# Optimization experiments

Hardware: AMD Instinct MI355X
Metric: run time of the kernel (lower is better)

## Reference

```python
import jax, jax.numpy as jnp
import numpy as np
import math

B, N, D, H, BS = 1, 2048, 1024, 16, 256  # batch, seq, d_model, heads, block_size


def setup_inputs() -> dict:
    key = jax.random.key(0)
    ks = jax.random.split(key, 8)
    s = 0.02  # init scale for projection weights
    return {
        "x": jax.random.normal(ks[0], (B, N, D), jnp.float32),
        "distance_bias": jax.random.uniform(ks[1], (N, N), dtype=jnp.float32),
        "Wq": jax.random.normal(ks[2], (D, D), jnp.float32) * s,
        "bq": jnp.zeros((D,), jnp.float32),
        "Wk": jax.random.normal(ks[3], (D, D), jnp.float32) * s,
        "bk": jnp.zeros((D,), jnp.float32),
        "Wv": jax.random.normal(ks[4], (D, D), jnp.float32) * s,
        "bv": jnp.zeros((D,), jnp.float32),
        "Wo": jax.random.normal(ks[5], (D, D), jnp.float32) * s,
        "bo": jnp.zeros((D,), jnp.float32),
    }


def reference(x, distance_bias, Wq, bq, Wk, bk, Wv, bv, Wo, bo):
    Bm, Nm, Dm = x.shape
    dk = Dm // H
    scale = 1.0 / math.sqrt(dk)
    nb = Nm // BS  # number of blocks along sequence

    def proj(W, b):
        # torch Linear: x @ W.T + b, then split heads -> [B, H, N, dk]
        return (x @ W.T + b).reshape(Bm, Nm, H, dk).transpose(0, 2, 1, 3)

    Q, K, V = proj(Wq, bq), proj(Wk, bk), proj(Wv, bv)

    # scores with toroidal bias subtracted (matches `scores - bias_block`)
    scores = jnp.einsum('bhqd,bhkd->bhqk', Q, K) * scale - distance_bias[None, None]
    # view as [B, H, n_qblk, BS, n_kblk, BS] and softmax PER (q-block, k-block)
    s6 = scores.reshape(Bm, H, nb, BS, nb, BS)
    w = jax.nn.softmax(s6, axis=-1)  # softmax over keys within each kv block

    Vb = V.reshape(Bm, H, nb, BS, dk)
    # sum over all kv blocks of (per-block softmax) @ V_block
    num = jnp.einsum('bhqsnk,bhnkd->bhqsd', w, Vb)  # [B,H,nb,BS,dk]
    # accumulated normalizer = sum of per-block softmax weights over all kv blocks
    norm = jnp.sum(w, axis=(4, 5))  # [B,H,nb,BS]
    O = num / (norm[..., None] + 1e-8)

    O = O.reshape(Bm, H, Nm, dk).transpose(0, 2, 1, 3).reshape(Bm, Nm, Dm)
    return O @ Wo.T + bo
```

## Files before the change

kernel.cpp:

```cpp
#include <hip/hip_runtime.h>
#include <hip/hip_fp16.h>

typedef _Float16 half8 __attribute__((ext_vector_type(8)));
typedef _Float16 half4v __attribute__((ext_vector_type(4)));
typedef float f32x4 __attribute__((ext_vector_type(4)));

#define NSEQ 2048
#define DMOD 1024
#define NHEAD 16
#define DK 64

#define GLOAD_LDS16(gp, lp) __builtin_amdgcn_global_load_lds(                 \
    (const __attribute__((address_space(1))) void*)(gp),                      \
    (__attribute__((address_space(3))) void*)(lp), 16, 0, 0)

#define WAIT_VM(n) (0xF70 | (n))


__global__ __launch_bounds__(256) void cast_pack(
    const float* __restrict__ x, const float* __restrict__ wq,
    const float* __restrict__ wk, const float* __restrict__ wv,
    const float* __restrict__ wo, const float* __restrict__ db,
    _Float16* __restrict__ dst, _Float16* __restrict__ bh)
{
    const int w = blockIdx.x * 4 + (threadIdx.x >> 6);
    const int ln = threadIdx.x & 63, m = ln & 15, qd = ln >> 4;
    if (w >= 12288) {
        const int loc = w - 12288;
        const int ks = loc >> 9;
        const int rem = loc & 511;
        const int q0g = rem >> 2;
        const int t2 = rem & 3;
#pragma unroll
        for (int tt = 0; tt < 2; ++tt) {
            const int t = t2 * 2 + tt;
            const float* p = db + (size_t)(q0g * 16 + m) * 2048
                             + ks * 128 + t * 16 + qd * 4;
            float4 a = *(const float4*)p;
            half4v h;
            h[0] = (_Float16)a.x; h[1] = (_Float16)a.y;
            h[2] = (_Float16)a.z; h[3] = (_Float16)a.w;
            *(half4v*)(bh + ((((size_t)ks * 128 + q0g) * 8 + t) * 64 + ln) * 4) = h;
        }
        return;
    }
    const float* src; _Float16* d; int loc;
    if (w < 4096) { src = x; d = dst; loc = w; }
    else {
        const int w2 = w - 4096, mat = w2 >> 11;
        loc = w2 & 2047;
        src = mat == 0 ? wq : mat == 1 ? wk : mat == 2 ? wv : wo;
        d = dst + 2097152 + mat * 1048576;
    }
    const int st = loc >> 5, kc = loc & 31;
    const float* p = src + (size_t)(st * 16 + m) * 1024 + kc * 32 + qd * 8;
    float4 a = *(const float4*)p, b = *(const float4*)(p + 4);
    half8 h;
    h[0] = (_Float16)a.x; h[1] = (_Float16)a.y; h[2] = (_Float16)a.z; h[3] = (_Float16)a.w;
    h[4] = (_Float16)b.x; h[5] = (_Float16)b.y; h[6] = (_Float16)b.z; h[7] = (_Float16)b.w;
    *(half8*)(d + (size_t)(loc * 64 + ln) * 8) = h;
}

__global__ __launch_bounds__(256) void cvt_bias(
    const float* __restrict__ db, _Float16* __restrict__ bh)
{
    const int w = blockIdx.x * 4 + (threadIdx.x >> 6);
    const int ln = threadIdx.x & 63, m = ln & 15, qd = ln >> 4;
    const int ks = w >> 9;
    const int rem = w & 511;
    const int q0g = rem >> 2;
    const int t2 = rem & 3;
#pragma unroll
    for (int tt = 0; tt < 2; ++tt) {
        const int t = t2 * 2 + tt;
        const float* p = db + (size_t)(q0g * 16 + m) * 2048
                         + ks * 128 + t * 16 + qd * 4;
        float4 a = *(const float4*)p;
        half4v h;
        h[0] = (_Float16)a.x; h[1] = (_Float16)a.y;
        h[2] = (_Float16)a.z; h[3] = (_Float16)a.w;
        *(half4v*)(bh + ((((size_t)ks * 128 + q0g) * 8 + t) * 64 + ln) * 4) = h;
    }
}

template<int BM, int BN, int BK, int MODE>
__global__ __launch_bounds__(256) void tgemm(
    const _Float16* __restrict__ A, const _Float16* __restrict__ A2,
    const _Float16* __restrict__ W0, const _Float16* __restrict__ W1,
    const _Float16* __restrict__ W2,
    const float* __restrict__ b0, const float* __restrict__ b1,
    const float* __restrict__ b2,
    _Float16* __restrict__ oQ, _Float16* __restrict__ oK,
    _Float16* __restrict__ oV, float* __restrict__ oF)
{
    constexpr int MT = BM / 32, NT = BN / 32;
    constexpr int KC = BK / 32;
    constexpr int NSTEP = 1024 / BK;
    constexpr int NAc = BM / 64, NBc = BN / 64;
    constexpr int SDMA = KC * ((MODE == 1 ? 2 * NAc : NAc) + NBc);
    __shared__ _Float16 sA[2 * BM * BK];
    __shared__ _Float16 sA2[MODE == 1 ? 2 * BM * BK : 1];
    __shared__ _Float16 sB[2 * BN * BK];
    const int tid = threadIdx.x, wv = tid >> 6, ln = tid & 63;
    const int m = ln & 15, qd = ln >> 4;
    const int row0 = blockIdx.x * BM;

    int sel = 0, colbase;
    const _Float16* W; const float* bias;
    if constexpr (MODE == 0) {
        sel = blockIdx.y >> 3;
        colbase = (blockIdx.y & 7) * BN;
        W = sel == 0 ? W0 : sel == 1 ? W1 : W2;
        bias = sel == 0 ? b0 : sel == 1 ? b1 : b2;
    } else {
        colbase = blockIdx.y * BN;
        W = W0; bias = b0;
    }
    const int wr = wv >> 1, wc = wv & 1;

    f32x4 acc[MT][NT];
#pragma unroll
    for (int i = 0; i < MT; ++i)
#pragma unroll
        for (int j = 0; j < NT; ++j) acc[i][j] = (f32x4){0.f, 0.f, 0.f, 0.f};

    auto stage = [&](int s, int b) {
        _Float16* dA = sA + b * (BM * BK);
        _Float16* dB = sB + b * (BN * BK);
#pragma unroll
        for (int c = 0; c < KC; ++c) {
            const int kc = s * KC + c;
#pragma unroll
            for (int ra = 0; ra < NAc; ++ra) {
                const int st = ra * 4 + wv;
                GLOAD_LDS16(A + ((size_t)((row0 >> 4) + st) * 32 + kc) * 512 + ln * 8,
                            dA + (c * (BM / 16) + st) * 512);
                if constexpr (MODE == 1) {
                    _Float16* dA2 = sA2 + b * (BM * BK);
                    GLOAD_LDS16(A2 + ((size_t)((row0 >> 4) + st) * 32 + kc) * 512 + ln * 8,
                                dA2 + (c * (BM / 16) + st) * 512);
                }
            }
#pragma unroll
            for (int rb = 0; rb < NBc; ++rb) {
                const int st = rb * 4 + wv;
                GLOAD_LDS16(W + ((size_t)((colbase >> 4) + st) * 32 + kc) * 512 + ln * 8,
                            dB + (c * (BN / 16) + st) * 512);
            }
        }
    };
    auto step = [&](int b) {
#pragma unroll
        for (int c = 0; c < KC; ++c) {
            const _Float16* cA = sA + b * (BM * BK) + c * (BM * 32);
            const _Float16* cB = sB + b * (BN * BK) + c * (BN * 32);
            half8 af[MT], bf[NT];
#pragma unroll
            for (int i = 0; i < MT; ++i) {
                const int off = ((wr * MT + i) * 64 + ln) * 8;
                if constexpr (MODE == 1) {
                    const _Float16* cA2 = sA2 + b * (BM * BK) + c * (BM * 32);
                    half8 xv = *(const half8*)(cA + off);
                    half8 yv = *(const half8*)(cA2 + off);
                    af[i] = xv + yv;
                } else {
                    af[i] = *(const half8*)(cA + off);
                }
            }
#pragma unroll
            for (int j = 0; j < NT; ++j)
                bf[j] = *(const half8*)(cB + ((wc * NT + j) * 64 + ln) * 8);
#pragma unroll
            for (int i = 0; i < MT; ++i)
#pragma unroll
                for (int j = 0; j < NT; ++j)
                    acc[i][j] = __builtin_amdgcn_mfma_f32_16x16x32_f16(af[i], bf[j], acc[i][j], 0, 0, 0);
        }
    };

    stage(0, 0);
#pragma unroll
    for (int s = 0; s < NSTEP; ++s) {
        if (s) __builtin_amdgcn_s_barrier();
        if (s + 1 < NSTEP) {
            stage(s + 1, (s + 1) & 1);
            __builtin_amdgcn_s_waitcnt(WAIT_VM(SDMA));
        } else {
            __builtin_amdgcn_s_waitcnt(WAIT_VM(0));
        }
        __builtin_amdgcn_s_barrier();
        step(s & 1);
    }

#pragma unroll
    for (int j = 0; j < NT; ++j) {
        const int col = colbase + wc * (BN / 2) + j * 16 + m;
        const float bv = bias[col];
#pragma unroll
        for (int i = 0; i < MT; ++i) {
            const int crow0 = row0 + wr * (BM / 2) + i * 16 + qd * 4;
            if constexpr (MODE == 1) {
#pragma unroll
                for (int r = 0; r < 4; ++r)
                    oF[(size_t)(crow0 + r) * DMOD + col] = acc[i][j][r] + bv;
            } else {
                const int h = col >> 6, d = col & 63;
                if (sel == 0) {
#pragma unroll
                    for (int r = 0; r < 4; ++r)
                        oQ[h * (NSEQ * DK) + (crow0 + r) * DK + d] =
                            (_Float16)((acc[i][j][r] + bv) * 0.125f);
                } else if (sel == 1) {
#pragma unroll
                    for (int r = 0; r < 4; ++r) {
                        const int n = crow0 + r;
                        oK[(size_t)(((h * 16 + (n >> 7)) * 16
                                     + ((n >> 4) & 7) * 2 + (d >> 5)) * 64
                                    + (n & 15) + 16 * ((d >> 3) & 3)) * 8
                           + (d & 7)] = (_Float16)(acc[i][j][r] + bv);
                    }
                } else {
                    half4v hv;
#pragma unroll
                    for (int r = 0; r < 4; ++r) hv[r] = (_Float16)(acc[i][j][r] + bv);
                    const int n0 = crow0;
                    *(half4v*)(oV + (size_t)(((h * 16 + (n0 >> 7)) * 16
                                              + ((n0 >> 5) & 3) * 4 + ((d >> 4) & 3)) * 64
                                             + (d & 15) + 16 * ((n0 >> 3) & 3)) * 8
                               + (n0 & 7)) = hv;
                }
            }
        }
    }
}

__global__ __launch_bounds__(512, 4) void attn(
    const _Float16* __restrict__ Q, const _Float16* __restrict__ Kt,
    const _Float16* __restrict__ Vt, const _Float16* __restrict__ bias_h,
    _Float16* __restrict__ Op)
{
    __shared__ _Float16 sK[8192];
    __shared__ _Float16 sV[8192];
    __shared__ _Float16 sP[16384];
    const int tid = threadIdx.x, wv = tid >> 6, ln = tid & 63;
    const int m = ln & 15, qd = ln >> 4;
    const int h = blockIdx.x;
    const int q0 = blockIdx.y * 128 + wv * 16;
    const int q0g = blockIdx.y * 8 + wv;
    const int kvb = blockIdx.z * 8;
    const _Float16* Qh = Q + h * (NSEQ * DK);
    const _Float16* Kh = Kt + h * (NSEQ * DK) + kvb * 8192;
    const _Float16* Vh = Vt + h * (NSEQ * DK) + kvb * 8192;
    const _Float16* bbase = bias_h + ((size_t)kvb * 128 + q0g) * 2048 + ln * 4;

    half8 qf[2];
    qf[0] = *(const half8*)(Qh + (q0 + m) * DK + qd * 8);
    qf[1] = *(const half8*)(Qh + (q0 + m) * DK + 32 + qd * 8);

    f32x4 oacc[4], oU[4];
#pragma unroll
    for (int v = 0; v < 4; ++v) {
        oacc[v] = (f32x4){0.f, 0.f, 0.f, 0.f};
        oU[v]   = (f32x4){0.f, 0.f, 0.f, 0.f};
    }
    float bsum = 0.f;

    for (int ls = 0; ls < 8; ++ls) {
        if (ls) __syncthreads();
        GLOAD_LDS16(Kh + ls * 8192 + wv * 512 + ln * 8, sK + wv * 512);
        GLOAD_LDS16(Kh + ls * 8192 + (wv + 8) * 512 + ln * 8, sK + (wv + 8) * 512);
        GLOAD_LDS16(Vh + ls * 8192 + wv * 512 + ln * 8, sV + wv * 512);
        GLOAD_LDS16(Vh + ls * 8192 + (wv + 8) * 512 + ln * 8, sV + (wv + 8) * 512);
        half4v bcur[8];
#pragma unroll
        for (int t = 0; t < 8; ++t)
            bcur[t] = *(const half4v*)(bbase + (size_t)ls * 262144 + t * 256);
        __syncthreads();

#pragma unroll
        for (int t = 0; t < 8; ++t) {
            half8 kf0 = *(const half8*)(sK + ((t * 2 + 0) * 64 + ln) * 8);
            half8 kf1 = *(const half8*)(sK + ((t * 2 + 1) * 64 + ln) * 8);
            f32x4 s = {0.f, 0.f, 0.f, 0.f};
            s = __builtin_amdgcn_mfma_f32_16x16x32_f16(kf0, qf[0], s, 0, 0, 0);
            s = __builtin_amdgcn_mfma_f32_16x16x32_f16(kf1, qf[1], s, 0, 0, 0);
            float p0 = __expf(s[0] - (float)bcur[t][0]);
            float p1 = __expf(s[1] - (float)bcur[t][1]);
            float p2 = __expf(s[2] - (float)bcur[t][2]);
            float p3 = __expf(s[3] - (float)bcur[t][3]);
            bsum += (p0 + p1) + (p2 + p3);
            half4v ph;
            ph[0] = (_Float16)p0; ph[1] = (_Float16)p1;
            ph[2] = (_Float16)p2; ph[3] = (_Float16)p3;
            *(half4v*)(sP + wv * 2048 + (t >> 1) * 512
                       + (((t & 1) * 2 + (qd >> 1)) * 16 + m) * 8
                       + (qd & 1) * 4) = ph;
        }

#pragma unroll
        for (int kk = 0; kk < 4; ++kk) {
            half8 pa = *(const half8*)(sP + wv * 2048 + kk * 512 + ln * 8);
#pragma unroll
            for (int vt = 0; vt < 4; ++vt) {
                half8 vb = *(const half8*)(sV + ((kk * 4 + vt) * 64 + ln) * 8);
                oU[vt] = __builtin_amdgcn_mfma_f32_16x16x32_f16(pa, vb, oU[vt], 0, 0, 0);
            }
        }

        if (ls & 1) {
            float s2 = bsum;
            s2 += __shfl_xor(s2, 16, 64);
            s2 += __shfl_xor(s2, 32, 64);
            float inv = 1.0f / (8.0f * s2);
            float iv[4];
#pragma unroll
            for (int r = 0; r < 4; ++r) iv[r] = __shfl(inv, qd * 4 + r, 64);
#pragma unroll
            for (int vt = 0; vt < 4; ++vt) {
#pragma unroll
                for (int r = 0; r < 4; ++r) oacc[vt][r] += iv[r] * oU[vt][r];
                oU[vt] = (f32x4){0.f, 0.f, 0.f, 0.f};
            }
            bsum = 0.f;
        }
    }

    _Float16* Opz = Op + (size_t)blockIdx.z * 2097152;
    const int st = q0g;
#pragma unroll
    for (int vt = 0; vt < 4; ++vt) {
        const int d = h * 64 + vt * 16 + m;
        _Float16* base = Opz + (size_t)(st * 32 + (d >> 5)) * 512
                         + ((d >> 3) & 3) * 128 + (d & 7);
#pragma unroll
        for (int r = 0; r < 4; ++r)
            base[(qd * 4 + r) * 8] = (_Float16)oacc[vt][r];
    }
}

extern "C" void kernel_launch(void* const* d_in, const int* in_sizes, int n_in,
                              void* d_out, int out_size, void* d_ws, size_t ws_size,
                              hipStream_t stream)
{
    const float* x  = (const float*)d_in[0];
    const float* db = (const float*)d_in[1];
    const float* Wq = (const float*)d_in[2];
    const float* bq = (const float*)d_in[3];
    const float* Wk = (const float*)d_in[4];
    const float* bk = (const float*)d_in[5];
    const float* Wv = (const float*)d_in[6];
    const float* bv = (const float*)d_in[7];
    const float* Wo = (const float*)d_in[8];
    const float* bo = (const float*)d_in[9];
    float* out = (float*)d_out;

    _Float16* ws  = (_Float16*)d_ws;
    _Float16* xh  = ws;
    _Float16* wqh = xh  + 2097152;
    _Float16* wkh = wqh + 1048576;
    _Float16* wvh = wkh + 1048576;
    _Float16* woh = wvh + 1048576;
    _Float16* Qb  = woh + 1048576;
    _Float16* Kb  = Qb  + 2097152;
    _Float16* Vtb = Kb  + 2097152;
    _Float16* Oh0 = Vtb + 2097152;
    _Float16* Oh1 = Oh0 + 2097152;

    const bool big_ws = ws_size >= (size_t)41943040;
    _Float16* bh = big_ws ? (Oh1 + 2097152) : ws;

    cast_pack<<<big_ws ? 5120 : 3072, 256, 0, stream>>>(
        x, Wq, Wk, Wv, Wo, db, xh, bh);

    tgemm<64, 128, 64, 0><<<dim3(32, 24), 256, 0, stream>>>(
        xh, nullptr, wqh, wkh, wvh, bq, bk, bv, Qb, Kb, Vtb, nullptr);

    if (!big_ws)
        cvt_bias<<<2048, 256, 0, stream>>>(db, bh);

    attn<<<dim3(NHEAD, NSEQ / 128, 2), 512, 0, stream>>>(Qb, Kb, Vtb, bh, Oh0);

    tgemm<64, 64, 64, 1><<<dim3(32, 16), 256, 0, stream>>>(
        Oh0, Oh1, woh, nullptr, nullptr, bo, nullptr, nullptr,
        nullptr, nullptr, nullptr, out);
}
```

Measured before the change: 162.1 us.

## Double-buffer K/V LDS tiles and prefetch bias in attention loop

The attention kernel's K/V shared-memory tiles become double-buffered, and the bias fragments are prefetched one stage ahead. The global loads for the next stage are issued before computing the current one, with an explicit vmcnt wait and raw barriers replacing the load-then-sync pattern. The aim is to overlap global memory latency with MFMA and exp work. In exchange, LDS use grows from 64KB to 96KB per block and launch bounds drop from 4 to 2 blocks, which lowers occupancy.

```diff
diff --git a/kernel.cpp b/kernel.cpp
--- a/kernel.cpp
+++ b/kernel.cpp
@@ -15,6 +15,8 @@
     (__attribute__((address_space(3))) void*)(lp), 16, 0, 0)
 
 #define WAIT_VM(n) (0xF70 | (n))
+
+template<bool B> struct Bc { static constexpr bool value = B; };
 
 
 __global__ __launch_bounds__(256) void cast_pack(
@@ -234,13 +236,13 @@
     }
 }
 
-__global__ __launch_bounds__(512, 4) void attn(
+__global__ __launch_bounds__(512, 2) void attn(
     const _Float16* __restrict__ Q, const _Float16* __restrict__ Kt,
     const _Float16* __restrict__ Vt, const _Float16* __restrict__ bias_h,
     _Float16* __restrict__ Op)
 {
-    __shared__ _Float16 sK[8192];
-    __shared__ _Float16 sV[8192];
+    __shared__ _Float16 sK[2][8192];
+    __shared__ _Float16 sV[2][8192];
     __shared__ _Float16 sP[16384];
     const int tid = threadIdx.x, wv = tid >> 6, ln = tid & 63;
     const int m = ln & 15, qd = ln >> 4;
@@ -265,29 +267,46 @@
     }
     float bsum = 0.f;
 
-    for (int ls = 0; ls < 8; ++ls) {
-        if (ls) __syncthreads();
-        GLOAD_LDS16(Kh + ls * 8192 + wv * 512 + ln * 8, sK + wv * 512);
-        GLOAD_LDS16(Kh + ls * 8192 + (wv + 8) * 512 + ln * 8, sK + (wv + 8) * 512);
-        GLOAD_LDS16(Vh + ls * 8192 + wv * 512 + ln * 8, sV + wv * 512);
-        GLOAD_LDS16(Vh + ls * 8192 + (wv + 8) * 512 + ln * 8, sV + (wv + 8) * 512);
-        half4v bcur[8];
-#pragma unroll
-        for (int t = 0; t < 8; ++t)
-            bcur[t] = *(const half4v*)(bbase + (size_t)ls * 262144 + t * 256);
-        __syncthreads();
-
+    auto stageKV = [&](int ls, int b) {
+        GLOAD_LDS16(Kh + ls * 8192 + wv * 512 + ln * 8, sK[b] + wv * 512);
+        GLOAD_LDS16(Kh + ls * 8192 + (wv + 8) * 512 + ln * 8, sK[b] + (wv + 8) * 512);
+        GLOAD_LDS16(Vh + ls * 8192 + wv * 512 + ln * 8, sV[b] + wv * 512);
+        GLOAD_LDS16(Vh + ls * 8192 + (wv + 8) * 512 + ln * 8, sV[b] + (wv + 8) * 512);
+    };
+
+    half4v bA[8], bB[8];
+    stageKV(0, 0);
+#pragma unroll
+    for (int t = 0; t < 8; ++t)
+        bA[t] = *(const half4v*)(bbase + t * 256);
+
+    auto step = [&](int ls, half4v (&bc)[8], half4v (&bn)[8], auto lastc) {
+        constexpr bool LAST = decltype(lastc)::value;
+        if (ls) __builtin_amdgcn_s_barrier();
+        if constexpr (!LAST) {
+            stageKV(ls + 1, (ls + 1) & 1);
+#pragma unroll
+            for (int t = 0; t < 8; ++t)
+                bn[t] = *(const half4v*)(bbase + (size_t)(ls + 1) * 262144 + t * 256);
+            __builtin_amdgcn_s_waitcnt(WAIT_VM(12));
+        } else {
+            __builtin_amdgcn_s_waitcnt(WAIT_VM(0));
+        }
+        __builtin_amdgcn_s_barrier();
+
+        const _Float16* sKc = sK[ls & 1];
+        const _Float16* sVc = sV[ls & 1];
 #pragma unroll
         for (int t = 0; t < 8; ++t) {
-            half8 kf0 = *(const half8*)(sK + ((t * 2 + 0) * 64 + ln) * 8);
-            half8 kf1 = *(const half8*)(sK + ((t * 2 + 1) * 64 + ln) * 8);
+            half8 kf0 = *(const half8*)(sKc + ((t * 2 + 0) * 64 + ln) * 8);
+            half8 kf1 = *(const half8*)(sKc + ((t * 2 + 1) * 64 + ln) * 8);
             f32x4 s = {0.f, 0.f, 0.f, 0.f};
             s = __builtin_amdgcn_mfma_f32_16x16x32_f16(kf0, qf[0], s, 0, 0, 0);
             s = __builtin_amdgcn_mfma_f32_16x16x32_f16(kf1, qf[1], s, 0, 0, 0);
-            float p0 = __expf(s[0] - (float)bcur[t][0]);
-            float p1 = __expf(s[1] - (float)bcur[t][1]);
-            float p2 = __expf(s[2] - (float)bcur[t][2]);
-            float p3 = __expf(s[3] - (float)bcur[t][3]);
+            float p0 = __expf(s[0] - (float)bc[t][0]);
+            float p1 = __expf(s[1] - (float)bc[t][1]);
+            float p2 = __expf(s[2] - (float)bc[t][2]);
+            float p3 = __expf(s[3] - (float)bc[t][3]);
             bsum += (p0 + p1) + (p2 + p3);
             half4v ph;
             ph[0] = (_Float16)p0; ph[1] = (_Float16)p1;
@@ -302,7 +321,7 @@
             half8 pa = *(const half8*)(sP + wv * 2048 + kk * 512 + ln * 8);
 #pragma unroll
             for (int vt = 0; vt < 4; ++vt) {
-                half8 vb = *(const half8*)(sV + ((kk * 4 + vt) * 64 + ln) * 8);
+                half8 vb = *(const half8*)(sVc + ((kk * 4 + vt) * 64 + ln) * 8);
                 oU[vt] = __builtin_amdgcn_mfma_f32_16x16x32_f16(pa, vb, oU[vt], 0, 0, 0);
             }
         }
@@ -323,7 +342,16 @@
             }
             bsum = 0.f;
         }
-    }
+    };
+
+    step(0, bA, bB, Bc<false>{});
+    step(1, bB, bA, Bc<false>{});
+    step(2, bA, bB, Bc<false>{});
+    step(3, bB, bA, Bc<false>{});
+    step(4, bA, bB, Bc<false>{});
+    step(5, bB, bA, Bc<false>{});
+    step(6, bA, bB, Bc<false>{});
+    step(7, bB, bA, Bc<true>{});
 
     _Float16* Opz = Op + (size_t)blockIdx.z * 2097152;
     const int st = q0g;
```

New measurement: 167.9 us. 3.6% more time.
